# Performance work log

Measured on AMD Instinct MI355X. Metric: run time of the kernel, lower is better.

The kernel has to match this reference:

```python
import jax, jax.numpy as jnp
import numpy as np

CK = 64  # key channels, used for the 1/sqrt(ck) scale


def setup_inputs() -> dict:
    key = jax.random.key(0)
    ks = jax.random.split(key, 9)
    B, C, D, H, W = 2, 64, 20, 20, 20
    ck = cv = co = 64
    s = 0.02
    return {
        "x": jax.random.normal(ks[0], (B, C, D, H, W), dtype=jnp.float32),
        "wq": jax.random.normal(ks[1], (ck, C), dtype=jnp.float32) * s,
        "bq": jax.random.normal(ks[2], (ck,), dtype=jnp.float32) * s,
        "wk": jax.random.normal(ks[3], (ck, C), dtype=jnp.float32) * s,
        "bk": jax.random.normal(ks[4], (ck,), dtype=jnp.float32) * s,
        "wv": jax.random.normal(ks[5], (cv, C), dtype=jnp.float32) * s,
        "bv": jax.random.normal(ks[6], (cv,), dtype=jnp.float32) * s,
        "wo": jax.random.normal(ks[7], (co, cv), dtype=jnp.float32) * s,
        "bo": jax.random.normal(ks[8], (co,), dtype=jnp.float32) * s,
    }


def reference(x, wq, bq, wk, bk, wv, bv, wo, bo):
    B, C, D, H, W = x.shape
    ck = wq.shape[0]
    cv = wv.shape[0]
    xf = x.reshape(B, C, -1)  # (B, C, N) with N = D*H*W
    # 1x1x1 convs == per-voxel channel matmuls
    q = jnp.einsum('kc,bcn->bnk', wq, xf) + bq           # (B, N, ck) queries (already transposed)
    k = jnp.einsum('kc,bcn->bkn', wk, xf) + bk[:, None]  # (B, ck, N) keys
    v = jnp.einsum('vc,bcn->bnv', wv, xf) + bv           # (B, N, cv) values (transposed)
    scale = 1.0 / jnp.sqrt(jnp.asarray(CK, dtype=x.dtype))
    attn = jax.nn.softmax(jnp.einsum('bnk,bkm->bnm', q, k) * scale, axis=-1)  # (B, N, N)
    # dropout is identity in eval mode
    out = jnp.einsum('bnm,bmv->bnv', attn, v)  # (B, N, cv)
    # faithful to torch: .view(batch, cv, d, h, w) reinterprets memory, no transpose
    out = out.reshape(B, cv, D, H, W)
    out = jnp.einsum('oc,bcdhw->bodhw', wo, out) + bo[None, :, None, None, None]
    return out
```

## Files before the change

### kernel.cpp

```cpp
#include <hip/hip_runtime.h>
#include <hip/hip_bf16.h>

typedef __bf16 bf16_t;
typedef __bf16 bf16x8 __attribute__((ext_vector_type(8)));
typedef float f32x4 __attribute__((ext_vector_type(4)));
typedef float f32x16 __attribute__((ext_vector_type(16)));
typedef unsigned uint2v __attribute__((ext_vector_type(2)));

#define NV 8000
#define QB 125

__device__ __forceinline__ bf16x8 cvt_bf16x8(const float* __restrict__ p) {
    float4 a = *reinterpret_cast<const float4*>(p);
    float4 b = *reinterpret_cast<const float4*>(p + 4);
    bf16x8 r;
    r[0] = (bf16_t)a.x; r[1] = (bf16_t)a.y; r[2] = (bf16_t)a.z; r[3] = (bf16_t)a.w;
    r[4] = (bf16_t)b.x; r[5] = (bf16_t)b.y; r[6] = (bf16_t)b.z; r[7] = (bf16_t)b.w;
    return r;
}

__device__ __forceinline__ unsigned pack2(float a, float b) {
    union { bf16_t h[2]; unsigned u; } x;
    x.h[0] = (bf16_t)a; x.h[1] = (bf16_t)b;
    return x.u;
}

__device__ __forceinline__ int sigma_of(int n) {
    int c = n / 125, a = n - 125 * c;
    return a * 64 + c;
}

__global__ __launch_bounds__(256) void qkv_kernel(
    const float* __restrict__ x,
    const float* __restrict__ wq, const float* __restrict__ bq,
    const float* __restrict__ wk, const float* __restrict__ bk,
    const float* __restrict__ wv, const float* __restrict__ bv,
    bf16_t* __restrict__ Q, bf16_t* __restrict__ Kr, bf16_t* __restrict__ Vt)
{
    __shared__ __align__(16) char xb[16 * 128];

    const int tid = threadIdx.x;
    const int b  = blockIdx.x / 500;
    const int n0 = (blockIdx.x % 500) * 16;

    {
        int c = tid >> 2, seg = tid & 3;
        float4 v4 = *reinterpret_cast<const float4*>(&x[((size_t)b * 64 + c) * NV + n0 + seg * 4]);
        #pragma unroll
        for (int j = 0; j < 4; ++j) {
            int vx = seg * 4 + j;
            *reinterpret_cast<bf16_t*>(xb + vx * 128 + ((c * 2) ^ ((vx & 7) << 4))) =
                (bf16_t)((&v4.x)[j]);
        }
    }
    __syncthreads();

    const int w  = tid >> 6;
    const int lane = tid & 63;
    const int g  = lane >> 4;
    const int lr = lane & 15;

    const bf16x8 xa0 = *reinterpret_cast<const bf16x8*>(
        xb + lr * 128 + ((16 * g) ^ ((lr & 7) << 4)));
    const bf16x8 xa1 = *reinterpret_cast<const bf16x8*>(
        xb + lr * 128 + ((64 + 16 * g) ^ ((lr & 7) << 4)));

    const f32x4 zero4 = {0.f, 0.f, 0.f, 0.f};
    const float QSCALE = 0.125f * 1.44269504088896f;
    const int kout = w * 16 + lr;

    {
        bf16x8 wb0 = cvt_bf16x8(wq + kout * 64 + 8 * g);
        bf16x8 wb1 = cvt_bf16x8(wq + kout * 64 + 32 + 8 * g);
        f32x4 acc = __builtin_amdgcn_mfma_f32_16x16x32_bf16(xa0, wb0, zero4, 0, 0, 0);
        acc = __builtin_amdgcn_mfma_f32_16x16x32_bf16(xa1, wb1, acc, 0, 0, 0);
        const float bias = bq[kout];
        #pragma unroll
        for (int j = 0; j < 4; ++j) {
            const int sig = sigma_of(n0 + 4 * g + j);
            Q[((size_t)b * NV + sig) * 64 + kout] = (bf16_t)((acc[j] + bias) * QSCALE);
        }
    }
    {
        bf16x8 wb0 = cvt_bf16x8(wk + kout * 64 + 8 * g);
        bf16x8 wb1 = cvt_bf16x8(wk + kout * 64 + 32 + 8 * g);
        f32x4 acc = __builtin_amdgcn_mfma_f32_16x16x32_bf16(xa0, wb0, zero4, 0, 0, 0);
        acc = __builtin_amdgcn_mfma_f32_16x16x32_bf16(xa1, wb1, acc, 0, 0, 0);
        const float bias = bk[kout];
        #pragma unroll
        for (int j = 0; j < 4; ++j)
            Kr[((size_t)b * NV + n0 + 4 * g + j) * 64 + kout] = (bf16_t)(acc[j] + bias);
    }
    {
        bf16x8 wb0 = cvt_bf16x8(wv + kout * 64 + 8 * g);
        bf16x8 wb1 = cvt_bf16x8(wv + kout * 64 + 32 + 8 * g);
        f32x4 acc = __builtin_amdgcn_mfma_f32_16x16x32_bf16(xa0, wb0, zero4, 0, 0, 0);
        acc = __builtin_amdgcn_mfma_f32_16x16x32_bf16(xa1, wb1, acc, 0, 0, 0);
        const float bias = bv[kout];
        union { uint2 u2; bf16_t h[4]; } pk;
        #pragma unroll
        for (int j = 0; j < 4; ++j) pk.h[j] = (bf16_t)(acc[j] + bias);
        *reinterpret_cast<uint2*>(&Vt[((size_t)b * 64 + kout) * NV + n0 + 4 * g]) = pk.u2;
    }
}

template<int S>
__global__ __launch_bounds__(256) void attn_kernel(
    const bf16_t* __restrict__ Q, const bf16_t* __restrict__ Kr,
    const bf16_t* __restrict__ Vt, bf16_t* __restrict__ Op, float* __restrict__ ml)
{
    __shared__ __align__(16) char kt[2][8192];
    __shared__ __align__(16) char vt[2][8192];

    const int tid  = threadIdx.x;
    const int s    = blockIdx.x % S;
    const int rem  = blockIdx.x / S;
    const int b    = rem / 63;
    const int qb   = rem % 63;
    const int q0   = qb * 128;
    const int t0   = (125 * s) / S;
    const int t1   = (125 * (s + 1)) / S;
    const int w    = tid >> 6;
    const int lane = tid & 63;
    const int lo   = lane & 31;
    const int hi   = lane >> 5;

    const int q  = q0 + w * 32 + lo;
    const int qc = q < NV ? q : NV - 1;

    bf16x8 bqf[4];
    {
        const bf16_t* qrow = Q + ((size_t)b * NV + qc) * 64 + hi * 8;
        #pragma unroll
        for (int kk = 0; kk < 4; ++kk)
            bqf[kk] = *reinterpret_cast<const bf16x8*>(qrow + kk * 16);
    }

    const char* kp = (const char*)(Kr + (size_t)b * NV * 64);
    const char* vp = (const char*)(Vt + (size_t)b * 64 * NV);

    const int gk0 = w, gk1 = w + 4;
    const size_t koff0 = (size_t)((gk0 >> 2) * 32 + lo) * 128 + (gk0 & 3) * 32 + hi * 16;
    const size_t koff1 = (size_t)((gk1 >> 2) * 32 + lo) * 128 + (gk1 & 3) * 32 + hi * 16;
    const size_t voff0 = (size_t)((gk0 & 1) * 32 + lo) * (NV * 2) + (size_t)((gk0 >> 1) * 16 + hi * 8) * 2;
    const size_t voff1 = (size_t)((gk1 & 1) * 32 + lo) * (NV * 2) + (size_t)((gk1 >> 1) * 16 + hi * 8) * 2;
    const int dst0 = gk0 * 1024 + lane * 16;
    const int dst1 = gk1 * 1024 + lane * 16;

    uint4 rk0_, rk1_, rv0_, rv1_;
#define ATTN_GLOB(m0) do { \
    rk0_ = *reinterpret_cast<const uint4*>(kp + (size_t)(m0) * 128 + koff0); \
    rk1_ = *reinterpret_cast<const uint4*>(kp + (size_t)(m0) * 128 + koff1); \
    rv0_ = *reinterpret_cast<const uint4*>(vp + (size_t)(m0) * 2 + voff0); \
    rv1_ = *reinterpret_cast<const uint4*>(vp + (size_t)(m0) * 2 + voff1); } while (0)
#define ATTN_DSW(bufi) do { \
    *reinterpret_cast<uint4*>(kt[bufi] + dst0) = rk0_; \
    *reinterpret_cast<uint4*>(kt[bufi] + dst1) = rk1_; \
    *reinterpret_cast<uint4*>(vt[bufi] + dst0) = rv0_; \
    *reinterpret_cast<uint4*>(vt[bufi] + dst1) = rv1_; } while (0)
#define ATTN_QK(bufi, dst) do { \
    const char* ktb_ = kt[bufi]; \
    _Pragma("unroll") \
    for (int kb = 0; kb < 2; ++kb) { \
        f32x16 acc_{}; \
        _Pragma("unroll") \
        for (int kk = 0; kk < 4; ++kk) { \
            const bf16x8 ka_ = *reinterpret_cast<const bf16x8*>( \
                ktb_ + ((kb * 4 + kk) * 64 + lane) * 16); \
            acc_ = __builtin_amdgcn_mfma_f32_32x32x16_bf16(ka_, bqf[kk], acc_, 0, 0, 0); \
        } \
        dst[kb] = acc_; } } while (0)

    f32x16 acco[2]; acco[0] = f32x16{}; acco[1] = f32x16{};
    float m = -1e30f, l = 0.f;

    const int nt = t1 - t0;
    ATTN_GLOB(t0 * 64); ATTN_DSW(0);
    if (nt > 1) { ATTN_GLOB((t0 + 1) * 64); ATTN_DSW(1); }
    if (nt > 2) ATTN_GLOB((t0 + 2) * 64);
    __syncthreads();

    f32x16 sa[2], sa2[2];
    ATTN_QK(0, sa);

    for (int t = t0; t < t1; ++t) {
        const int p = (t - t0) & 1;

        if (t + 1 < t1) ATTN_QK(p ^ 1, sa2);

        float mx;
        {
            float v8[8];
            #pragma unroll
            for (int r = 0; r < 8; ++r)
                v8[r] = fmaxf(fmaxf(sa[0][r], sa[0][r + 8]),
                              fmaxf(sa[1][r], sa[1][r + 8]));
            float v4a = fmaxf(v8[0], v8[4]), v4b = fmaxf(v8[1], v8[5]);
            float v4c = fmaxf(v8[2], v8[6]), v4d = fmaxf(v8[3], v8[7]);
            mx = fmaxf(fmaxf(v4a, v4b), fmaxf(v4c, v4d));
        }
        {
            union { float f; unsigned u; } xu; xu.f = mx;
            uint2v r = __builtin_amdgcn_permlane32_swap(xu.u, xu.u, false, false);
            union { unsigned u; float f; } po; po.u = hi ? r[0] : r[1];
            mx = fmaxf(mx, po.f);
        }
        if (__any(mx > m + 8.0f)) {
            const float mn2 = fmaxf(m, mx);
            const float corr = exp2f(m - mn2);
            m = mn2;
            l *= corr;
            acco[0] *= corr;
            acco[1] *= corr;
        }

        float ps = 0.f;
        unsigned Uw[2][4][2];
        #pragma unroll
        for (int kb = 0; kb < 2; ++kb) {
            #pragma unroll
            for (int j = 0; j < 4; ++j) {
                float p0 = exp2f(sa[kb][4 * j + 0] - m);
                float p1 = exp2f(sa[kb][4 * j + 1] - m);
                float p2 = exp2f(sa[kb][4 * j + 2] - m);
                float p3 = exp2f(sa[kb][4 * j + 3] - m);
                ps += (p0 + p1) + (p2 + p3);
                Uw[kb][j][0] = pack2(p0, p1);
                Uw[kb][j][1] = pack2(p2, p3);
            }
        }
        {
            union { float f; unsigned u; } xu; xu.f = ps;
            uint2v r = __builtin_amdgcn_permlane32_swap(xu.u, xu.u, false, false);
            union { unsigned u; float f; } po; po.u = hi ? r[0] : r[1];
            ps += po.f;
        }
        l += ps;

        const char* vtb = vt[p];
        #pragma unroll
        for (int kb = 0; kb < 2; ++kb) {
            #pragma unroll
            for (int e = 0; e < 2; ++e) {
                uint2v r0 = __builtin_amdgcn_permlane32_swap(
                    Uw[kb][2 * e][0], Uw[kb][2 * e + 1][0], false, false);
                uint2v r1 = __builtin_amdgcn_permlane32_swap(
                    Uw[kb][2 * e][1], Uw[kb][2 * e + 1][1], false, false);
                union { unsigned u[4]; bf16x8 v; } pf;
                pf.u[0] = r0[0]; pf.u[1] = r1[0];
                pf.u[2] = r0[1]; pf.u[3] = r1[1];
                const int ks = kb * 2 + e;
                #pragma unroll
                for (int vb = 0; vb < 2; ++vb) {
                    const bf16x8 va = *reinterpret_cast<const bf16x8*>(
                        vtb + ((ks * 2 + vb) * 64 + lane) * 16);
                    acco[vb] = __builtin_amdgcn_mfma_f32_32x32x16_bf16(va, pf.v, acco[vb], 0, 0, 0);
                }
            }
        }

        __syncthreads();
        if (t + 2 < t1) ATTN_DSW(p);
        __syncthreads();
        if (t + 3 < t1) ATTN_GLOB((t + 3) * 64);
        if (t + 1 < t1) { sa[0] = sa2[0]; sa[1] = sa2[1]; }
    }

    if (q < NV) {
        const size_t obase = ((size_t)(s * 2 + b) * NV + q) * 64;
        #pragma unroll
        for (int vb = 0; vb < 2; ++vb) {
            #pragma unroll
            for (int j = 0; j < 4; ++j) {
                union { uint2 u2; bf16_t h[4]; } pk;
                #pragma unroll
                for (int i = 0; i < 4; ++i) pk.h[i] = (bf16_t)acco[vb][4 * j + i];
                *reinterpret_cast<uint2*>(&Op[obase + vb * 32 + 8 * j + 4 * hi]) = pk.u2;
            }
        }
        if (hi == 0) {
            float2 t2; t2.x = m; t2.y = l;
            *reinterpret_cast<float2*>(&ml[((size_t)(s * 2 + b) * NV + q) * 2]) = t2;
        }
    }
#undef ATTN_GLOB
#undef ATTN_DSW
#undef ATTN_QK
}

template<int S>
__global__ __launch_bounds__(256) void projc_kernel(
    const bf16_t* __restrict__ Op, const float* __restrict__ ml,
    const float* __restrict__ wo, const float* __restrict__ bo,
    float* __restrict__ out)
{
    __shared__ __align__(16) char bt[16 * 128];
    __shared__ float al[64 * 8];

    const int tid = threadIdx.x;
    const int b   = blockIdx.x / 500;
    const int rem = blockIdx.x % 500;
    const int a   = rem >> 2;
    const int nf  = rem & 3;

    if (tid < 64) {
        const int row = a * 64 + tid;
        float M = -1e30f;
        #pragma unroll
        for (int s = 0; s < S; ++s)
            M = fmaxf(M, ml[((size_t)(s * 2 + b) * NV + row) * 2]);
        float L = 0.f, av[S];
        #pragma unroll
        for (int s = 0; s < S; ++s) {
            const float mm = ml[((size_t)(s * 2 + b) * NV + row) * 2];
            const float ll = ml[((size_t)(s * 2 + b) * NV + row) * 2 + 1];
            const float aa = exp2f(mm - M);
            L += ll * aa;
            av[s] = aa;
        }
        const float inv = 1.0f / L;
        #pragma unroll
        for (int s = 0; s < S; ++s) al[tid * 8 + s] = av[s] * inv;
    }
    __syncthreads();

    {
        const int c = tid >> 2, sg = tid & 3;
        f32x4 acc = {0.f, 0.f, 0.f, 0.f};
        #pragma unroll
        for (int s = 0; s < S; ++s) {
            const float fac = al[c * 8 + s];
            union { uint2 u2; bf16_t h[4]; } cv;
            cv.u2 = *reinterpret_cast<const uint2*>(
                &Op[((size_t)(s * 2 + b) * NV + a * 64 + c) * 64 + nf * 16 + sg * 4]);
            #pragma unroll
            for (int j = 0; j < 4; ++j) acc[j] += fac * (float)cv.h[j];
        }
        #pragma unroll
        for (int j = 0; j < 4; ++j) {
            const int v = sg * 4 + j;
            *reinterpret_cast<bf16_t*>(bt + v * 128 + ((c * 2) ^ ((v & 7) << 4))) =
                (bf16_t)acc[j];
        }
    }
    __syncthreads();

    const int w  = tid >> 6;
    const int lane = tid & 63;
    const int g  = lane >> 4;
    const int lr = lane & 15;

    const int orow = w * 16 + lr;
    const bf16x8 wa0 = cvt_bf16x8(wo + orow * 64 + 8 * g);
    const bf16x8 wa1 = cvt_bf16x8(wo + orow * 64 + 32 + 8 * g);
    const float4 bo4 = *reinterpret_cast<const float4*>(&bo[w * 16 + 4 * g]);

    const f32x4 zero4 = {0.f, 0.f, 0.f, 0.f};
    const bf16x8 gb0 = *reinterpret_cast<const bf16x8*>(
        bt + lr * 128 + ((16 * g) ^ ((lr & 7) << 4)));
    const bf16x8 gb1 = *reinterpret_cast<const bf16x8*>(
        bt + lr * 128 + ((64 + 16 * g) ^ ((lr & 7) << 4)));
    f32x4 acc = __builtin_amdgcn_mfma_f32_16x16x32_bf16(wa0, gb0, zero4, 0, 0, 0);
    acc = __builtin_amdgcn_mfma_f32_16x16x32_bf16(wa1, gb1, acc, 0, 0, 0);
    #pragma unroll
    for (int j = 0; j < 4; ++j) {
        const int o = w * 16 + 4 * g + j;
        out[((size_t)b * 64 + o) * NV + a * 64 + nf * 16 + lr] = acc[j] + (&bo4.x)[j];
    }
}

extern "C" void kernel_launch(void* const* d_in, const int* in_sizes, int n_in,
                              void* d_out, int out_size, void* d_ws, size_t ws_size,
                              hipStream_t stream)
{
    const float* x  = (const float*)d_in[0];
    const float* wq = (const float*)d_in[1];
    const float* bq = (const float*)d_in[2];
    const float* wk = (const float*)d_in[3];
    const float* bk = (const float*)d_in[4];
    const float* wv = (const float*)d_in[5];
    const float* bv = (const float*)d_in[6];
    const float* wo = (const float*)d_in[7];
    const float* bo = (const float*)d_in[8];
    float* out = (float*)d_out;

    char* ws = (char*)d_ws;
    bf16_t* Q  = (bf16_t*)(ws);
    bf16_t* Kr = (bf16_t*)(ws + 2048000);
    bf16_t* Vt = (bf16_t*)(ws + 4096000);

    int S = 8;
    if (ws_size < 6144000ull + 8ull * 2176000ull) S = 4;
    if (ws_size < 6144000ull + 4ull * 2176000ull) S = 2;
    if (ws_size < 6144000ull + 2ull * 2176000ull) S = 1;

    bf16_t* Op = (bf16_t*)(ws + 6144000);
    float*  ml = (float*)(ws + 6144000 + (size_t)S * 2048000);

    qkv_kernel<<<dim3(2 * 500), dim3(256), 0, stream>>>(x, wq, bq, wk, bk, wv, bv, Q, Kr, Vt);

    if (S == 8) {
        attn_kernel<8><<<dim3(8 * 2 * 63), dim3(256), 0, stream>>>(Q, Kr, Vt, Op, ml);
        projc_kernel<8><<<dim3(2 * 500), dim3(256), 0, stream>>>(Op, ml, wo, bo, out);
    } else if (S == 4) {
        attn_kernel<4><<<dim3(4 * 2 * 63), dim3(256), 0, stream>>>(Q, Kr, Vt, Op, ml);
        projc_kernel<4><<<dim3(2 * 500), dim3(256), 0, stream>>>(Op, ml, wo, bo, out);
    } else if (S == 2) {
        attn_kernel<2><<<dim3(2 * 2 * 63), dim3(256), 0, stream>>>(Q, Kr, Vt, Op, ml);
        projc_kernel<2><<<dim3(2 * 500), dim3(256), 0, stream>>>(Op, ml, wo, bo, out);
    } else {
        attn_kernel<1><<<dim3(1 * 2 * 63), dim3(256), 0, stream>>>(Q, Kr, Vt, Op, ml);
        projc_kernel<1><<<dim3(2 * 500), dim3(256), 0, stream>>>(Op, ml, wo, bo, out);
    }
}
```

Before: 175.6 us.

## Use single-wave attention blocks loading K/V straight into registers

The attention kernel now runs one 64-thread wave per block and loads K and V fragments directly from global memory into registers, with a software prefetch of the next tile. This removes the shared-memory staging and both per-iteration __syncthreads. Block order is remapped so the split index and batch vary fastest, which may improve L2 sharing of K/V across waves. The default split count drops from 8 to 4. In exchange, K/V global traffic rises fourfold because each wave fetches its own copy instead of sharing a block-wide tile, and register pressure grows.

```diff
diff --git a/kernel.cpp b/kernel.cpp
--- a/kernel.cpp
+++ b/kernel.cpp
@@ -105,23 +105,21 @@
 }
 
 template<int S>
-__global__ __launch_bounds__(256) void attn_kernel(
+__global__ __launch_bounds__(64) void attn_kernel(
     const bf16_t* __restrict__ Q, const bf16_t* __restrict__ Kr,
     const bf16_t* __restrict__ Vt, bf16_t* __restrict__ Op, float* __restrict__ ml)
 {
-    __shared__ __align__(16) char kt[2][8192];
-    __shared__ __align__(16) char vt[2][8192];
-
-    const int tid  = threadIdx.x;
-    const int s    = blockIdx.x % S;
-    const int rem  = blockIdx.x / S;
-    const int b    = rem / 63;
-    const int qb   = rem % 63;
+    const int bid  = blockIdx.x;
+    const int grp  = bid % (2 * S);
+    const int s    = grp >> 1;
+    const int b    = grp & 1;
+    const int j    = bid / (2 * S);
+    const int qb   = j >> 2;
+    const int w    = j & 3;
     const int q0   = qb * 128;
     const int t0   = (125 * s) / S;
     const int t1   = (125 * (s + 1)) / S;
-    const int w    = tid >> 6;
-    const int lane = tid & 63;
+    const int lane = threadIdx.x & 63;
     const int lo   = lane & 31;
     const int hi   = lane >> 5;
 
@@ -138,55 +136,54 @@
 
     const char* kp = (const char*)(Kr + (size_t)b * NV * 64);
     const char* vp = (const char*)(Vt + (size_t)b * 64 * NV);
-
-    const int gk0 = w, gk1 = w + 4;
-    const size_t koff0 = (size_t)((gk0 >> 2) * 32 + lo) * 128 + (gk0 & 3) * 32 + hi * 16;
-    const size_t koff1 = (size_t)((gk1 >> 2) * 32 + lo) * 128 + (gk1 & 3) * 32 + hi * 16;
-    const size_t voff0 = (size_t)((gk0 & 1) * 32 + lo) * (NV * 2) + (size_t)((gk0 >> 1) * 16 + hi * 8) * 2;
-    const size_t voff1 = (size_t)((gk1 & 1) * 32 + lo) * (NV * 2) + (size_t)((gk1 >> 1) * 16 + hi * 8) * 2;
-    const int dst0 = gk0 * 1024 + lane * 16;
-    const int dst1 = gk1 * 1024 + lane * 16;
-
-    uint4 rk0_, rk1_, rv0_, rv1_;
-#define ATTN_GLOB(m0) do { \
-    rk0_ = *reinterpret_cast<const uint4*>(kp + (size_t)(m0) * 128 + koff0); \
-    rk1_ = *reinterpret_cast<const uint4*>(kp + (size_t)(m0) * 128 + koff1); \
-    rv0_ = *reinterpret_cast<const uint4*>(vp + (size_t)(m0) * 2 + voff0); \
-    rv1_ = *reinterpret_cast<const uint4*>(vp + (size_t)(m0) * 2 + voff1); } while (0)
-#define ATTN_DSW(bufi) do { \
-    *reinterpret_cast<uint4*>(kt[bufi] + dst0) = rk0_; \
-    *reinterpret_cast<uint4*>(kt[bufi] + dst1) = rk1_; \
-    *reinterpret_cast<uint4*>(vt[bufi] + dst0) = rv0_; \
-    *reinterpret_cast<uint4*>(vt[bufi] + dst1) = rv1_; } while (0)
-#define ATTN_QK(bufi, dst) do { \
-    const char* ktb_ = kt[bufi]; \
-    _Pragma("unroll") \
-    for (int kb = 0; kb < 2; ++kb) { \
-        f32x16 acc_{}; \
-        _Pragma("unroll") \
-        for (int kk = 0; kk < 4; ++kk) { \
-            const bf16x8 ka_ = *reinterpret_cast<const bf16x8*>( \
-                ktb_ + ((kb * 4 + kk) * 64 + lane) * 16); \
-            acc_ = __builtin_amdgcn_mfma_f32_32x32x16_bf16(ka_, bqf[kk], acc_, 0, 0, 0); \
-        } \
+    const char* kptr  = kp + (size_t)t0 * 8192 + lo * 128 + hi * 16;
+    const char* vptr0 = vp + (size_t)lo * (NV * 2) + (size_t)t0 * 128 + hi * 16;
+    const char* vptr1 = vptr0 + (size_t)32 * (NV * 2);
+
+    bf16x8 kr[2][4];
+    bf16x8 vr[2][4];
+
+#define ATTN_LOADK() do {                                                       \
+    _Pragma("unroll")                                                           \
+    for (int kb = 0; kb < 2; ++kb)                                              \
+        _Pragma("unroll")                                                       \
+        for (int kk = 0; kk < 4; ++kk)                                          \
+            kr[kb][kk] = *reinterpret_cast<const bf16x8*>(kptr + kb * 4096 + kk * 32); \
+    kptr += 8192; } while (0)
+
+#define ATTN_LOADV() do {                                                       \
+    _Pragma("unroll")                                                           \
+    for (int ks = 0; ks < 4; ++ks) {                                            \
+        vr[0][ks] = *reinterpret_cast<const bf16x8*>(vptr0 + ks * 32);          \
+        vr[1][ks] = *reinterpret_cast<const bf16x8*>(vptr1 + ks * 32);          \
+    }                                                                           \
+    vptr0 += 128; vptr1 += 128; } while (0)
+
+#define ATTN_QK(dst) do {                                                       \
+    _Pragma("unroll")                                                           \
+    for (int kb = 0; kb < 2; ++kb) {                                            \
+        f32x16 acc_{};                                                          \
+        _Pragma("unroll")                                                       \
+        for (int kk = 0; kk < 4; ++kk)                                          \
+            acc_ = __builtin_amdgcn_mfma_f32_32x32x16_bf16(kr[kb][kk], bqf[kk], acc_, 0, 0, 0); \
         dst[kb] = acc_; } } while (0)
 
     f32x16 acco[2]; acco[0] = f32x16{}; acco[1] = f32x16{};
     float m = -1e30f, l = 0.f;
 
     const int nt = t1 - t0;
-    ATTN_GLOB(t0 * 64); ATTN_DSW(0);
-    if (nt > 1) { ATTN_GLOB((t0 + 1) * 64); ATTN_DSW(1); }
-    if (nt > 2) ATTN_GLOB((t0 + 2) * 64);
-    __syncthreads();
-
     f32x16 sa[2], sa2[2];
-    ATTN_QK(0, sa);
+
+    ATTN_LOADK();
+    ATTN_LOADV();
+    ATTN_QK(sa);
+    if (nt > 1) ATTN_LOADK();
 
     for (int t = t0; t < t1; ++t) {
-        const int p = (t - t0) & 1;
-
-        if (t + 1 < t1) ATTN_QK(p ^ 1, sa2);
+        if (t + 1 < t1) {
+            ATTN_QK(sa2);
+            if (t + 2 < t1) ATTN_LOADK();
+        }
 
         float mx;
         {
@@ -219,14 +216,14 @@
         #pragma unroll
         for (int kb = 0; kb < 2; ++kb) {
             #pragma unroll
-            for (int j = 0; j < 4; ++j) {
-                float p0 = exp2f(sa[kb][4 * j + 0] - m);
-                float p1 = exp2f(sa[kb][4 * j + 1] - m);
-                float p2 = exp2f(sa[kb][4 * j + 2] - m);
-                float p3 = exp2f(sa[kb][4 * j + 3] - m);
+            for (int jj = 0; jj < 4; ++jj) {
+                float p0 = exp2f(sa[kb][4 * jj + 0] - m);
+                float p1 = exp2f(sa[kb][4 * jj + 1] - m);
+                float p2 = exp2f(sa[kb][4 * jj + 2] - m);
+                float p3 = exp2f(sa[kb][4 * jj + 3] - m);
                 ps += (p0 + p1) + (p2 + p3);
-                Uw[kb][j][0] = pack2(p0, p1);
-                Uw[kb][j][1] = pack2(p2, p3);
+                Uw[kb][jj][0] = pack2(p0, p1);
+                Uw[kb][jj][1] = pack2(p2, p3);
             }
         }
         {
@@ -237,7 +234,6 @@
         }
         l += ps;
 
-        const char* vtb = vt[p];
         #pragma unroll
         for (int kb = 0; kb < 2; ++kb) {
             #pragma unroll
@@ -251,19 +247,16 @@
                 pf.u[2] = r0[1]; pf.u[3] = r1[1];
                 const int ks = kb * 2 + e;
                 #pragma unroll
-                for (int vb = 0; vb < 2; ++vb) {
-                    const bf16x8 va = *reinterpret_cast<const bf16x8*>(
-                        vtb + ((ks * 2 + vb) * 64 + lane) * 16);
-                    acco[vb] = __builtin_amdgcn_mfma_f32_32x32x16_bf16(va, pf.v, acco[vb], 0, 0, 0);
-                }
+                for (int vb = 0; vb < 2; ++vb)
+                    acco[vb] = __builtin_amdgcn_mfma_f32_32x32x16_bf16(
+                        vr[vb][ks], pf.v, acco[vb], 0, 0, 0);
             }
         }
 
-        __syncthreads();
-        if (t + 2 < t1) ATTN_DSW(p);
-        __syncthreads();
-        if (t + 3 < t1) ATTN_GLOB((t + 3) * 64);
-        if (t + 1 < t1) { sa[0] = sa2[0]; sa[1] = sa2[1]; }
+        if (t + 1 < t1) {
+            ATTN_LOADV();
+            sa[0] = sa2[0]; sa[1] = sa2[1];
+        }
     }
 
     if (q < NV) {
@@ -271,11 +264,11 @@
         #pragma unroll
         for (int vb = 0; vb < 2; ++vb) {
             #pragma unroll
-            for (int j = 0; j < 4; ++j) {
+            for (int jj = 0; jj < 4; ++jj) {
                 union { uint2 u2; bf16_t h[4]; } pk;
                 #pragma unroll
-                for (int i = 0; i < 4; ++i) pk.h[i] = (bf16_t)acco[vb][4 * j + i];
-                *reinterpret_cast<uint2*>(&Op[obase + vb * 32 + 8 * j + 4 * hi]) = pk.u2;
+                for (int i = 0; i < 4; ++i) pk.h[i] = (bf16_t)acco[vb][4 * jj + i];
+                *reinterpret_cast<uint2*>(&Op[obase + vb * 32 + 8 * jj + 4 * hi]) = pk.u2;
             }
         }
         if (hi == 0) {
@@ -283,8 +276,8 @@
             *reinterpret_cast<float2*>(&ml[((size_t)(s * 2 + b) * NV + q) * 2]) = t2;
         }
     }
-#undef ATTN_GLOB
-#undef ATTN_DSW
+#undef ATTN_LOADK
+#undef ATTN_LOADV
 #undef ATTN_QK
 }
 
@@ -334,13 +327,13 @@
             cv.u2 = *reinterpret_cast<const uint2*>(
                 &Op[((size_t)(s * 2 + b) * NV + a * 64 + c) * 64 + nf * 16 + sg * 4]);
             #pragma unroll
-            for (int j = 0; j < 4; ++j) acc[j] += fac * (float)cv.h[j];
-        }
-        #pragma unroll
-        for (int j = 0; j < 4; ++j) {
-            const int v = sg * 4 + j;
+            for (int jj = 0; jj < 4; ++jj) acc[jj] += fac * (float)cv.h[jj];
+        }
+        #pragma unroll
+        for (int jj = 0; jj < 4; ++jj) {
+            const int v = sg * 4 + jj;
             *reinterpret_cast<bf16_t*>(bt + v * 128 + ((c * 2) ^ ((v & 7) << 4))) =
-                (bf16_t)acc[j];
+                (bf16_t)acc[jj];
         }
     }
     __syncthreads();
@@ -363,9 +356,9 @@
     f32x4 acc = __builtin_amdgcn_mfma_f32_16x16x32_bf16(wa0, gb0, zero4, 0, 0, 0);
     acc = __builtin_amdgcn_mfma_f32_16x16x32_bf16(wa1, gb1, acc, 0, 0, 0);
     #pragma unroll
-    for (int j = 0; j < 4; ++j) {
-        const int o = w * 16 + 4 * g + j;
-        out[((size_t)b * 64 + o) * NV + a * 64 + nf * 16 + lr] = acc[j] + (&bo4.x)[j];
+    for (int jj = 0; jj < 4; ++jj) {
+        const int o = w * 16 + 4 * g + jj;
+        out[((size_t)b * 64 + o) * NV + a * 64 + nf * 16 + lr] = acc[jj] + (&bo4.x)[jj];
     }
 }
 
@@ -389,8 +382,7 @@
     bf16_t* Kr = (bf16_t*)(ws + 2048000);
     bf16_t* Vt = (bf16_t*)(ws + 4096000);
 
-    int S = 8;
-    if (ws_size < 6144000ull + 8ull * 2176000ull) S = 4;
+    int S = 4;
     if (ws_size < 6144000ull + 4ull * 2176000ull) S = 2;
     if (ws_size < 6144000ull + 2ull * 2176000ull) S = 1;
 
@@ -399,17 +391,14 @@
 
     qkv_kernel<<<dim3(2 * 500), dim3(256), 0, stream>>>(x, wq, bq, wk, bk, wv, bv, Q, Kr, Vt);
 
-    if (S == 8) {
-        attn_kernel<8><<<dim3(8 * 2 * 63), dim3(256), 0, stream>>>(Q, Kr, Vt, Op, ml);
-        projc_kernel<8><<<dim3(2 * 500), dim3(256), 0, stream>>>(Op, ml, wo, bo, out);
-    } else if (S == 4) {
-        attn_kernel<4><<<dim3(4 * 2 * 63), dim3(256), 0, stream>>>(Q, Kr, Vt, Op, ml);
+    if (S == 4) {
+        attn_kernel<4><<<dim3(4 * 2 * 252), dim3(64), 0, stream>>>(Q, Kr, Vt, Op, ml);
         projc_kernel<4><<<dim3(2 * 500), dim3(256), 0, stream>>>(Op, ml, wo, bo, out);
     } else if (S == 2) {
-        attn_kernel<2><<<dim3(2 * 2 * 63), dim3(256), 0, stream>>>(Q, Kr, Vt, Op, ml);
+        attn_kernel<2><<<dim3(2 * 2 * 252), dim3(64), 0, stream>>>(Q, Kr, Vt, Op, ml);
         projc_kernel<2><<<dim3(2 * 500), dim3(256), 0, stream>>>(Op, ml, wo, bo, out);
     } else {
-        attn_kernel<1><<<dim3(1 * 2 * 63), dim3(256), 0, stream>>>(Q, Kr, Vt, Op, ml);
+        attn_kernel<1><<<dim3(1 * 2 * 252), dim3(64), 0, stream>>>(Q, Kr, Vt, Op, ml);
         projc_kernel<1><<<dim3(2 * 500), dim3(256), 0, stream>>>(Op, ml, wo, bo, out);
     }
 }
```

New measurement: 208.1 us. +18.5%, slower.
